# Performance work log

Hardware: AMD Instinct MI355X
Metric: run time of the kernel (lower is better)

## Reference

```python
import math
import jax, jax.numpy as jnp
import numpy as np

B, S, HID, NH = 8, 512, 1024, 16
D = HID // NH          # head dim = 64
SPAN = 512             # att_span = max_relative_positions = max_position_embeddings


def _linear(x, W, b):
    # torch nn.Linear: y = x @ W.T + b, W is [out, in]
    return jnp.einsum('...i,oi->...o', x, W) + b


def _heads(x):
    # [B, S, HID] -> [B, NH, S, D]
    b, s, _ = x.shape
    return x.reshape(b, s, NH, D).transpose(0, 2, 1, 3)


def setup_inputs() -> dict:
    key = jax.random.key(0)
    ks = jax.random.split(key, 16)
    f = lambda i, shape, sc=1.0: jax.random.normal(ks[i], shape, dtype=jnp.float32) * sc
    return {
        'q': f(0, (B, S, HID)),
        'k': f(1, (B, S, HID)),
        'v': f(2, (B, S, HID)),
        'attention_mask': jnp.tril(jnp.ones((S, S), dtype=bool))[None, None],  # causal [1,1,S,S]
        'Wq': f(3, (HID, HID), 0.02), 'bq': jnp.zeros((HID,), jnp.float32),
        'Wk': f(4, (HID, HID), 0.02), 'bk': jnp.zeros((HID,), jnp.float32),
        'Wv': f(5, (HID, HID), 0.02), 'bv': jnp.zeros((HID,), jnp.float32),
        'Wpk': f(6, (HID, HID), 0.02), 'bpk': jnp.zeros((HID,), jnp.float32),
        'Wpq': f(7, (HID, HID), 0.02), 'bpq': jnp.zeros((HID,), jnp.float32),
        'rel_emb': f(8, (2 * SPAN, HID), 0.02),
    }


def reference(q, k, v, attention_mask, Wq, bq, Wk, bk, Wv, bv, Wpk, bpk, Wpq, bpq, rel_emb):
    scale_factor = 3  # 1 (content) + c2p + p2c
    scale = 1.0 / math.sqrt(D * scale_factor)

    ql = _heads(_linear(q, Wq, bq))   # [B,NH,S,D]
    kl = _heads(_linear(k, Wk, bk))
    vl = _heads(_linear(v, Wv, bv))

    # content-to-content scores
    scores = jnp.einsum('bhqd,bhkd->bhqk', ql, kl) * scale

    # relative positions (no bucketing since position_buckets = -1)
    rel = jnp.arange(S)[:, None] - jnp.arange(S)[None, :]          # [S,S]
    c2p_pos = jnp.clip(rel + SPAN, 0, 2 * SPAN - 1)
    p2c_pos = jnp.clip(-rel + SPAN, 0, 2 * SPAN - 1)

    # projected relative-position embeddings -> [NH, 2*SPAN, D]
    pk = _linear(rel_emb, Wpk, bpk).reshape(2 * SPAN, NH, D).transpose(1, 0, 2)
    pq = _linear(rel_emb, Wpq, bpq).reshape(2 * SPAN, NH, D).transpose(1, 0, 2)

    # content-to-position: out[b,h,q,k] = (q . pos_key)[b,h,q, c2p_pos[q,k]]
    c2p = jnp.einsum('bhqd,hjd->bhqj', ql, pk) * scale             # [B,NH,S,2*SPAN]
    c2p = jnp.take_along_axis(c2p, jnp.broadcast_to(c2p_pos[None, None], (B, NH, S, S)), axis=-1)

    # position-to-content: gathered[b,h,k,q] = (k . pos_query)[b,h,k, p2c_pos[k,q]], then transpose
    p2c = jnp.einsum('bhkd,hjd->bhkj', kl, pq) * scale             # [B,NH,S,2*SPAN]
    p2c = jnp.take_along_axis(p2c, jnp.broadcast_to(p2c_pos[None, None], (B, NH, S, S)), axis=-1)

    scores = scores + c2p + jnp.swapaxes(p2c, -1, -2)
    # subtract detached row max (as in torch: .max(...).values.detach())
    scores = scores - jax.lax.stop_gradient(scores.max(axis=-1, keepdims=True))

    # XSoftmax: masked softmax, then zero masked positions
    neg = jnp.float32(-1e30)
    probs = jax.nn.softmax(jnp.where(attention_mask, scores, neg), axis=-1)
    probs = jnp.where(attention_mask, probs, 0.0)

    ctx = jnp.einsum('bhqk,bhkd->bhqd', probs, vl)                 # [B,NH,S,D]
    return ctx.transpose(0, 2, 1, 3).reshape(B, S, HID)
```

## Files before the change

### kernel.cpp

```cpp
#include <hip/hip_runtime.h>
#include <hip/hip_bf16.h>
#include <math.h>

#define SCALE 0.07216878364870323f
#define NEG_BIG -1e30f

typedef __attribute__((ext_vector_type(8))) short bf16x8;
typedef __attribute__((ext_vector_type(4))) short bf16x4;
typedef __attribute__((ext_vector_type(4))) float f32x4;
#define MFMA_BF16 __builtin_amdgcn_mfma_f32_16x16x32_bf16

#define BARX()   asm volatile("s_barrier" ::: "memory")
#define VMCNT2() asm volatile("s_waitcnt vmcnt(2)" ::: "memory")
#define VMCNT0() asm volatile("s_waitcnt vmcnt(0)" ::: "memory")

static __device__ __forceinline__ float bf2f(__hip_bfloat16 x) { return __bfloat162float(x); }
static __device__ __forceinline__ __hip_bfloat16 f2bf(float x) { return __float2bfloat16(x); }
static __device__ __forceinline__ short f2bs(float x) {
  union { __hip_bfloat16 b; short s; } u; u.b = __float2bfloat16(x); return u.s;
}
static __device__ __forceinline__ float s2f(short v) {
  union { float f; unsigned u; } x; x.u = ((unsigned)(unsigned short)v) << 16; return x.f;
}
static __device__ __forceinline__ bf16x4 cvt4(float4 f) {
  bf16x4 r; r[0] = f2bs(f.x); r[1] = f2bs(f.y); r[2] = f2bs(f.z); r[3] = f2bs(f.w);
  return r;
}
static __device__ __forceinline__ bf16x8 ldg8(const __hip_bfloat16* p) {
  return *(const bf16x8*)p;
}
static __device__ __forceinline__ void gl_lds16(const __hip_bfloat16* g, __hip_bfloat16* l) {
  __builtin_amdgcn_global_load_lds(
      (const __attribute__((address_space(1))) void*)g,
      (__attribute__((address_space(3))) void*)l, 16, 0, 0);
}

struct CvtJob { const float* src; __hip_bfloat16* dst; int n4; };
struct CvtArgs { CvtJob j[9]; };

__global__ __launch_bounds__(256) void cvt_kernel(CvtArgs a) {
  const CvtJob jb = a.j[blockIdx.y];
  const float4* s = (const float4*)jb.src;
  bf16x4* d = (bf16x4*)jb.dst;
  const int stride = gridDim.x * 256;
  for (int i = blockIdx.x * 256 + threadIdx.x; i < jb.n4; i += stride)
    d[i] = cvt4(s[i]);
}

struct Gemm { const __hip_bfloat16* A; const __hip_bfloat16* W;
              const float* bias; __hip_bfloat16* out; int mode; int mBits; int nBlk;
              float oscale; };
struct ProjArgs { Gemm g[5]; };

static __device__ __forceinline__ void stage_half(const __hip_bfloat16* gtile,
                                                  __hip_bfloat16* ltile,
                                                  int half, int wave, int lane) {
  const int r = lane >> 3;
  const int chunk = (lane & 7) ^ r;
#pragma unroll
  for (int c = 0; c < 2; c++) {
    const int rowbase = half * 128 + c * 64 + wave * 8;
    gl_lds16(gtile + (size_t)(rowbase + r) * 1024 + chunk * 8,
             ltile + (size_t)rowbase * 64);
  }
}

__global__ __launch_bounds__(512, 2) void proj_kernel(ProjArgs pa) {
  const Gemm g = pa.g[blockIdx.y];
  if ((int)blockIdx.x >= g.nBlk) return;
  __shared__ __hip_bfloat16 As[2][256][64];
  __shared__ __hip_bfloat16 Ws[2][256][64];

  const int bid = blockIdx.x;
  const int m0 = (bid & ((1 << g.mBits) - 1)) * 256;
  const int n0 = (bid >> g.mBits) * 256;
  const int tid = threadIdx.x;
  const int wave = tid >> 6, lane = tid & 63;
  const int q16 = lane >> 4, l16 = lane & 15;
  const int wr = wave >> 2, wc = wave & 3;
  const int l7 = l16 & 7;

  const __hip_bfloat16* Ag = g.A + (size_t)m0 * 1024;
  const __hip_bfloat16* Wg = g.W + (size_t)n0 * 1024;

  f32x4 acc[8][4] = {};

  stage_half(Ag, &As[0][0][0], 0, wave, lane);
  stage_half(Ag, &As[0][0][0], 1, wave, lane);
  stage_half(Wg, &Ws[0][0][0], 0, wave, lane);
  stage_half(Wg, &Ws[0][0][0], 1, wave, lane);
  stage_half(Ag + 64, &As[1][0][0], 0, wave, lane);
  VMCNT2();
  BARX();

  for (int t = 0; t < 16; ++t) {
    const int cur = t & 1;
    const __hip_bfloat16* Ac = &As[cur][0][0];
    const __hip_bfloat16* Wc = &Ws[cur][0][0];
    __hip_bfloat16* An = &As[cur ^ 1][0][0];
    __hip_bfloat16* Wn = &Ws[cur ^ 1][0][0];
    const __hip_bfloat16* gAn = Ag + (size_t)(t + 1) * 64;
    const __hip_bfloat16* gWn = Wg + (size_t)(t + 1) * 64;
    const bool pf = (t + 1 < 16);

#pragma unroll
    for (int kh = 0; kh < 2; kh++) {
      const int csw = ((kh * 4 + q16) ^ l7) * 8;
      bf16x8 bw[4];
#pragma unroll
      for (int ni = 0; ni < 4; ni++)
        bw[ni] = *(const bf16x8*)(Wc + (size_t)(wc * 64 + ni * 16 + l16) * 64 + csw);
#pragma unroll
      for (int mh = 0; mh < 2; mh++) {
        bf16x8 af[4];
#pragma unroll
        for (int mi = 0; mi < 4; mi++)
          af[mi] = *(const bf16x8*)(Ac + (size_t)(wr * 128 + mh * 64 + mi * 16 + l16) * 64 + csw);
        const int ph = kh * 2 + mh;
        if (pf) {
          if (ph == 0)      stage_half(gAn, An, 1, wave, lane);
          else if (ph == 1) stage_half(gWn, Wn, 0, wave, lane);
          else if (ph == 2) stage_half(gWn, Wn, 1, wave, lane);
        }
        __builtin_amdgcn_s_setprio(1);
#pragma unroll
        for (int ni = 0; ni < 4; ni++)
#pragma unroll
          for (int mi = 0; mi < 4; mi++)
            acc[mh * 4 + mi][ni] =
                MFMA_BF16(af[mi], bw[ni], acc[mh * 4 + mi][ni], 0, 0, 0);
        __builtin_amdgcn_s_setprio(0);
      }
    }
    BARX();
    if (t + 2 < 16) {
      stage_half(Ag + (size_t)(t + 2) * 64, &As[cur][0][0], 0, wave, lane);
      VMCNT2();
    } else {
      VMCNT0();
    }
    BARX();
  }

#pragma unroll
  for (int ni = 0; ni < 4; ni++) {
    const int n = n0 + wc * 64 + ni * 16 + l16;
#pragma unroll
    for (int mi = 0; mi < 8; mi++) {
#pragma unroll
      for (int rr = 0; rr < 4; rr++) {
        const int m = m0 + wr * 128 + mi * 16 + q16 * 4 + rr;
        float val = acc[mi][ni][rr];
        size_t oidx;
        if (g.mode == 0) {
          val = (val + g.bias[n]) * g.oscale;
          const int b = m >> 9, s = m & 511;
          const int h = n >> 6, d = n & 63;
          oidx = ((size_t)((b * 16 + h) * 512 + s)) * 64 + d;
        } else if (g.mode == 1) {
          val = (val + g.bias[m]) * g.oscale;
          const int b = n >> 9, s = n & 511;
          const int h = m >> 6, d = m & 63;
          oidx = ((size_t)((b * 16 + h) * 64 + d)) * 512 + s;
        } else {
          val = (val + g.bias[n]) * g.oscale;
          const int h = n >> 6, d = n & 63;
          oidx = ((size_t)(h * 512 + m)) * 64 + d;
        }
        g.out[oidx] = f2bf(val);
      }
    }
  }
}

__global__ __launch_bounds__(256) void attn_kernel(
    const __hip_bfloat16* __restrict__ ql,
    const __hip_bfloat16* __restrict__ kl,
    const __hip_bfloat16* __restrict__ vlT,
    const __hip_bfloat16* __restrict__ pk,
    const __hip_bfloat16* __restrict__ pq,
    float* __restrict__ out)
{
  __shared__ __align__(16) __hip_bfloat16 pool[2][64][72];
  __shared__ __align__(16) __hip_bfloat16 pqs[2][32][72];
  __shared__ __align__(16) float qkbuf[32][36];
  __shared__ __align__(16) __hip_bfloat16 cpb[2][32][68];
  __shared__ __align__(16) __hip_bfloat16 pT[64][36];
  __shared__ __align__(16) __hip_bfloat16 ptile[32][40];
  __shared__ __align__(16) __hip_bfloat16 vt[64][40];
  __shared__ float mred[32];
  __shared__ float rsum[32];

  const int bid = blockIdx.x;
  const int qt = 15 - (bid >> 7);
  const int bh = bid & 127;
  const int h = bh & 15, b = bh >> 4;
  const int q0 = qt * 32;

  const __hip_bfloat16* qlp = ql + (size_t)bh * 512 * 64;
  const __hip_bfloat16* klp = kl + (size_t)bh * 512 * 64;
  const __hip_bfloat16* vtp = vlT + (size_t)bh * 64 * 512;
  const __hip_bfloat16* pkp = pk + (size_t)h * 512 * 64;
  const __hip_bfloat16* pqp = pq + (size_t)h * 512 * 64;

  const int tid = threadIdx.x, wave = tid >> 6, lane = tid & 63;
  const int q16 = lane >> 4, l16 = lane & 15;
  const int wr = wave & 1, wc = wave >> 1;

  bf16x8 qlB[2][2];
#pragma unroll
  for (int ksi = 0; ksi < 2; ksi++)
#pragma unroll
    for (int bq = 0; bq < 2; bq++)
      qlB[ksi][bq] = ldg8(qlp + (size_t)(q0 + bq * 16 + l16) * 64 + ksi * 32 + q16 * 8);

  {
    int4 z = {0, 0, 0, 0};
    *(int4*)(&pqs[1][tid >> 3][(tid & 7) * 8]) = z;
  }

  const int kEnd = q0 + 32;
  const int nIter = kEnd >> 5;

  const int sr = tid >> 3, sseg = tid & 7;
  const int vr = tid >> 2, vs = tid & 3;
  int4 rKv, rPKv, rPQv, rVt;
  {
    rKv  = ((const int4*)(klp + (size_t)(q0 + sr) * 64))[sseg];
    rPKv = ((const int4*)(pkp + (size_t)(0 + sr) * 64))[sseg];
    rPQv = ((const int4*)(pqp + (size_t)(0 + sr) * 64))[sseg];
    rVt  = ((const int4*)(vtp + (size_t)vr * 512 + q0))[vs];
  }

  const int aq = tid >> 3;
  const int kb = (tid & 7) * 4;
  float m_old = -INFINITY, s_part = 0.f;
  f32x4 octx[2] = {};

  for (int it = 0; it < nIter; ++it) {
    const int k0 = q0 - it * 32;
    const int par = it & 1;
    *(int4*)(&pool[par][sr][sseg * 8])      = rKv;
    *(int4*)(&pool[par][32 + sr][sseg * 8]) = rPKv;
    *(int4*)(&pqs[par][sr][sseg * 8])       = rPQv;
    if (it + 1 < nIter) {
      const int k0n = k0 - 32, jbn = (it + 1) * 32;
      rKv  = ((const int4*)(klp + (size_t)(k0n + sr) * 64))[sseg];
      rPKv = ((const int4*)(pkp + (size_t)(jbn + sr) * 64))[sseg];
      rPQv = ((const int4*)(pqp + (size_t)(jbn + sr) * 64))[sseg];
    }
    __syncthreads();

    const int arb = (wave == 1) ? 32 : 0;
    f32x4 a4[2][2] = {};
    __builtin_amdgcn_s_setprio(1);
#pragma unroll
    for (int ksi = 0; ksi < 2; ksi++) {
      const int ko = ksi * 32 + q16 * 8;
      bf16x8 Af0 = *(const bf16x8*)(&pool[par][arb + l16][ko]);
      bf16x8 Af1 = *(const bf16x8*)(&pool[par][arb + 16 + l16][ko]);
      bf16x8 Bf0, Bf1;
      if (wave < 2) {
        Bf0 = qlB[ksi][0];
        Bf1 = qlB[ksi][1];
      } else {
        const int ps = (wave == 2) ? (par ^ 1) : par;
        Bf0 = *(const bf16x8*)(&pqs[ps][l16][ko]);
        Bf1 = *(const bf16x8*)(&pqs[ps][16 + l16][ko]);
      }
      a4[0][0] = MFMA_BF16(Af0, Bf0, a4[0][0], 0, 0, 0);
      a4[0][1] = MFMA_BF16(Af0, Bf1, a4[0][1], 0, 0, 0);
      a4[1][0] = MFMA_BF16(Af1, Bf0, a4[1][0], 0, 0, 0);
      a4[1][1] = MFMA_BF16(Af1, Bf1, a4[1][1], 0, 0, 0);
    }
    __builtin_amdgcn_s_setprio(0);
    if (wave == 0) {
#pragma unroll
      for (int a = 0; a < 2; a++)
#pragma unroll
        for (int bq = 0; bq < 2; bq++)
          *(f32x4*)(&qkbuf[bq * 16 + l16][a * 16 + q16 * 4]) = a4[a][bq];
    } else if (wave == 1) {
#pragma unroll
      for (int a = 0; a < 2; a++)
#pragma unroll
        for (int bq = 0; bq < 2; bq++) {
          bf16x4 v;
#pragma unroll
          for (int r = 0; r < 4; r++) v[r] = f2bs(a4[a][bq][r]);
          const int q = bq * 16 + l16, jr = a * 16 + q16 * 4;
          *(bf16x4*)(&cpb[par][q][32 + jr]) = v;
          *(bf16x4*)(&cpb[par ^ 1][q][jr]) = v;
        }
    } else {
      const int rb = (wave == 3) ? 32 : 0;
#pragma unroll
      for (int a = 0; a < 2; a++)
#pragma unroll
        for (int bq = 0; bq < 2; bq++) {
          bf16x4 v;
#pragma unroll
          for (int r = 0; r < 4; r++) v[r] = f2bs(a4[a][bq][r]);
          *(bf16x4*)(&pT[rb + bq * 16 + l16][a * 16 + q16 * 4]) = v;
        }
    }
    __syncthreads();

    {
      const f32x4 qk4 = *(const f32x4*)(&qkbuf[aq][kb]);
      float v[4];
      float tmax = -INFINITY;
#pragma unroll
      for (int j = 0; j < 4; j++) {
        const int dlt = aq - (kb + j);
        v[j] = qk4[j] + bf2f(cpb[par][aq][dlt + 32]) + bf2f(pT[dlt + 32][kb + j]);
        if ((it == 0) && (dlt < 0)) v[j] = -INFINITY;
        else tmax = fmaxf(tmax, v[j]);
      }
      tmax = fmaxf(tmax, __shfl_xor(tmax, 1));
      tmax = fmaxf(tmax, __shfl_xor(tmax, 2));
      tmax = fmaxf(tmax, __shfl_xor(tmax, 4));
      const float m_new = fmaxf(m_old, tmax);
      const float f = __expf(m_old - m_new);
      bf16x4 pv4;
      float psum = 0.f;
#pragma unroll
      for (int j = 0; j < 4; j++) {
        const float p = __expf(v[j] - m_new);
        pv4[j] = f2bs(p);
        psum += p;
      }
      s_part = s_part * f + psum;
      m_old = m_new;
      *(bf16x4*)(&ptile[aq][kb]) = pv4;
      if ((tid & 7) == 0) mred[aq] = f;
    }
    {
      *(int4*)(&vt[vr][vs * 8]) = rVt;
      if (it + 1 < nIter)
        rVt = ((const int4*)(vtp + (size_t)vr * 512 + (k0 - 32)))[vs];
    }
    __syncthreads();

    {
      float fr[4];
#pragma unroll
      for (int rr = 0; rr < 4; rr++) fr[rr] = mred[wr * 16 + q16 * 4 + rr];
      bf16x8 af = *(const bf16x8*)(&ptile[wr * 16 + l16][q16 * 8]);
      __builtin_amdgcn_s_setprio(1);
#pragma unroll
      for (int cs = 0; cs < 2; cs++) {
        bf16x8 bv = *(const bf16x8*)(&vt[wc * 32 + cs * 16 + l16][q16 * 8]);
        f32x4 c = octx[cs];
#pragma unroll
        for (int rr = 0; rr < 4; rr++) c[rr] *= fr[rr];
        octx[cs] = MFMA_BF16(af, bv, c, 0, 0, 0);
      }
      __builtin_amdgcn_s_setprio(0);
    }
  }

  {
    float s = s_part;
    s += __shfl_xor(s, 1);
    s += __shfl_xor(s, 2);
    s += __shfl_xor(s, 4);
    if ((tid & 7) == 0) rsum[aq] = s;
  }
  __syncthreads();

  for (int cs = 0; cs < 2; cs++) {
    const int d = wc * 32 + cs * 16 + l16;
    for (int rr = 0; rr < 4; rr++) {
      const int qh = wr * 16 + q16 * 4 + rr;
      const float val = octx[cs][rr] / rsum[qh];
      out[((size_t)(b * 512 + q0 + qh)) * 1024 + h * 64 + d] = val;
    }
  }
}

extern "C" void kernel_launch(void* const* d_in, const int* in_sizes, int n_in,
                              void* d_out, int out_size, void* d_ws, size_t ws_size,
                              hipStream_t stream) {
  const float* q   = (const float*)d_in[0];
  const float* k   = (const float*)d_in[1];
  const float* v   = (const float*)d_in[2];
  const float* Wq  = (const float*)d_in[4];
  const float* bq  = (const float*)d_in[5];
  const float* Wk  = (const float*)d_in[6];
  const float* bk  = (const float*)d_in[7];
  const float* Wv  = (const float*)d_in[8];
  const float* bv  = (const float*)d_in[9];
  const float* Wpk = (const float*)d_in[10];
  const float* bpk = (const float*)d_in[11];
  const float* Wpq = (const float*)d_in[12];
  const float* bpq = (const float*)d_in[13];
  const float* rel = (const float*)d_in[14];
  float* out = (float*)d_out;

  char* ws = (char*)d_ws;
  const size_t MB = 1u << 20;
  __hip_bfloat16* bqi  = (__hip_bfloat16*)(ws);
  __hip_bfloat16* bki  = (__hip_bfloat16*)(ws + 8 * MB);
  __hip_bfloat16* bvi  = (__hip_bfloat16*)(ws + 16 * MB);
  __hip_bfloat16* bWq  = (__hip_bfloat16*)(ws + 24 * MB);
  __hip_bfloat16* bWk  = (__hip_bfloat16*)(ws + 26 * MB);
  __hip_bfloat16* bWv  = (__hip_bfloat16*)(ws + 28 * MB);
  __hip_bfloat16* bWpk = (__hip_bfloat16*)(ws + 30 * MB);
  __hip_bfloat16* bWpq = (__hip_bfloat16*)(ws + 32 * MB);
  __hip_bfloat16* brel = (__hip_bfloat16*)(ws + 34 * MB);
  __hip_bfloat16* wql  = (__hip_bfloat16*)(ws + 35 * MB);
  __hip_bfloat16* wkl  = (__hip_bfloat16*)(ws + 43 * MB);
  __hip_bfloat16* wvlT = (__hip_bfloat16*)(ws + 51 * MB);
  __hip_bfloat16* wpk  = (__hip_bfloat16*)(ws + 59 * MB);
  __hip_bfloat16* wpq  = (__hip_bfloat16*)(ws + 60 * MB);

  CvtArgs ca;
  ca.j[0] = { q,   bqi,  4194304 / 4 };
  ca.j[1] = { k,   bki,  4194304 / 4 };
  ca.j[2] = { v,   bvi,  4194304 / 4 };
  ca.j[3] = { Wq,  bWq,  1048576 / 4 };
  ca.j[4] = { Wk,  bWk,  1048576 / 4 };
  ca.j[5] = { Wv,  bWv,  1048576 / 4 };
  ca.j[6] = { Wpk, bWpk, 1048576 / 4 };
  ca.j[7] = { Wpq, bWpq, 1048576 / 4 };
  ca.j[8] = { rel + (size_t)512 * 1024, brel, 524288 / 4 };
  cvt_kernel<<<dim3(1024, 9), 256, 0, stream>>>(ca);

  ProjArgs pj;
  pj.g[0] = { bqi,  bWq,  bq,  wql,  0, 4, 64, SCALE };
  pj.g[1] = { bki,  bWk,  bk,  wkl,  0, 4, 64, 1.0f };
  pj.g[2] = { bWv,  bvi,  bv,  wvlT, 1, 2, 64, 1.0f };
  pj.g[3] = { brel, bWpk, bpk, wpk,  2, 1, 8,  1.0f };
  pj.g[4] = { brel, bWpq, bpq, wpq,  2, 1, 8,  SCALE };
  proj_kernel<<<dim3(64, 5), 512, 0, stream>>>(pj);

  attn_kernel<<<2048, 256, 0, stream>>>(wql, wkl, wvlT, wpk, wpq, out);
}
```

Before: 231.5 us.

## Restructure projection GEMM to 4-stage pipeline with 32-wide K slices

```diff
diff --git a/kernel.cpp b/kernel.cpp
--- a/kernel.cpp
+++ b/kernel.cpp
@@ -11,8 +11,11 @@
 #define MFMA_BF16 __builtin_amdgcn_mfma_f32_16x16x32_bf16
 
 #define BARX()   asm volatile("s_barrier" ::: "memory")
-#define VMCNT2() asm volatile("s_waitcnt vmcnt(2)" ::: "memory")
+#define VMCNT8() asm volatile("s_waitcnt vmcnt(8)" ::: "memory")
+#define VMCNT4() asm volatile("s_waitcnt vmcnt(4)" ::: "memory")
 #define VMCNT0() asm volatile("s_waitcnt vmcnt(0)" ::: "memory")
+#define LGKM0()  do { asm volatile("s_waitcnt lgkmcnt(0)" ::: "memory"); \
+                      __builtin_amdgcn_sched_barrier(0); } while (0)
 
 static __device__ __forceinline__ float bf2f(__hip_bfloat16 x) { return __bfloat162float(x); }
 static __device__ __forceinline__ __hip_bfloat16 f2bf(float x) { return __float2bfloat16(x); }
@@ -52,24 +55,24 @@
               float oscale; };
 struct ProjArgs { Gemm g[5]; };
 
-static __device__ __forceinline__ void stage_half(const __hip_bfloat16* gtile,
-                                                  __hip_bfloat16* ltile,
-                                                  int half, int wave, int lane) {
-  const int r = lane >> 3;
-  const int chunk = (lane & 7) ^ r;
+static __device__ __forceinline__ void stage32(const __hip_bfloat16* gpanel,
+                                               __hip_bfloat16* lslot,
+                                               int tt, int wave, int lane) {
+  const int rsub = lane >> 2;
+  const int chunk = lane & 3;
 #pragma unroll
   for (int c = 0; c < 2; c++) {
-    const int rowbase = half * 128 + c * 64 + wave * 8;
-    gl_lds16(gtile + (size_t)(rowbase + r) * 1024 + chunk * 8,
-             ltile + (size_t)rowbase * 64);
+    const int row = c * 128 + wave * 16 + rsub;
+    gl_lds16(gpanel + (size_t)row * 1024 + tt * 32 + chunk * 8,
+             lslot + (size_t)(c * 128 + wave * 16) * 32);
   }
 }
 
 __global__ __launch_bounds__(512, 2) void proj_kernel(ProjArgs pa) {
   const Gemm g = pa.g[blockIdx.y];
   if ((int)blockIdx.x >= g.nBlk) return;
-  __shared__ __hip_bfloat16 As[2][256][64];
-  __shared__ __hip_bfloat16 Ws[2][256][64];
+  __shared__ __hip_bfloat16 As[4][256][32];
+  __shared__ __hip_bfloat16 Ws[4][256][32];
 
   const int bid = blockIdx.x;
   const int m0 = (bid & ((1 << g.mBits) - 1)) * 256;
@@ -78,68 +81,71 @@
   const int wave = tid >> 6, lane = tid & 63;
   const int q16 = lane >> 4, l16 = lane & 15;
   const int wr = wave >> 2, wc = wave & 3;
-  const int l7 = l16 & 7;
 
   const __hip_bfloat16* Ag = g.A + (size_t)m0 * 1024;
   const __hip_bfloat16* Wg = g.W + (size_t)n0 * 1024;
 
   f32x4 acc[8][4] = {};
 
-  stage_half(Ag, &As[0][0][0], 0, wave, lane);
-  stage_half(Ag, &As[0][0][0], 1, wave, lane);
-  stage_half(Wg, &Ws[0][0][0], 0, wave, lane);
-  stage_half(Wg, &Ws[0][0][0], 1, wave, lane);
-  stage_half(Ag + 64, &As[1][0][0], 0, wave, lane);
-  VMCNT2();
+  stage32(Ag, &As[0][0][0], 0, wave, lane);
+  stage32(Wg, &Ws[0][0][0], 0, wave, lane);
+  stage32(Ag, &As[1][0][0], 1, wave, lane);
+  stage32(Wg, &Ws[1][0][0], 1, wave, lane);
+  stage32(Ag, &As[2][0][0], 2, wave, lane);
+  stage32(Wg, &Ws[2][0][0], 2, wave, lane);
+  VMCNT8();
   BARX();
 
-  for (int t = 0; t < 16; ++t) {
-    const int cur = t & 1;
-    const __hip_bfloat16* Ac = &As[cur][0][0];
-    const __hip_bfloat16* Wc = &Ws[cur][0][0];
-    __hip_bfloat16* An = &As[cur ^ 1][0][0];
-    __hip_bfloat16* Wn = &Ws[cur ^ 1][0][0];
-    const __hip_bfloat16* gAn = Ag + (size_t)(t + 1) * 64;
-    const __hip_bfloat16* gWn = Wg + (size_t)(t + 1) * 64;
-    const bool pf = (t + 1 < 16);
-
-#pragma unroll
-    for (int kh = 0; kh < 2; kh++) {
-      const int csw = ((kh * 4 + q16) ^ l7) * 8;
-      bf16x8 bw[4];
-#pragma unroll
-      for (int ni = 0; ni < 4; ni++)
-        bw[ni] = *(const bf16x8*)(Wc + (size_t)(wc * 64 + ni * 16 + l16) * 64 + csw);
-#pragma unroll
-      for (int mh = 0; mh < 2; mh++) {
-        bf16x8 af[4];
-#pragma unroll
-        for (int mi = 0; mi < 4; mi++)
-          af[mi] = *(const bf16x8*)(Ac + (size_t)(wr * 128 + mh * 64 + mi * 16 + l16) * 64 + csw);
-        const int ph = kh * 2 + mh;
-        if (pf) {
-          if (ph == 0)      stage_half(gAn, An, 1, wave, lane);
-          else if (ph == 1) stage_half(gWn, Wn, 0, wave, lane);
-          else if (ph == 2) stage_half(gWn, Wn, 1, wave, lane);
-        }
-        __builtin_amdgcn_s_setprio(1);
-#pragma unroll
-        for (int ni = 0; ni < 4; ni++)
-#pragma unroll
-          for (int mi = 0; mi < 4; mi++)
-            acc[mh * 4 + mi][ni] =
-                MFMA_BF16(af[mi], bw[ni], acc[mh * 4 + mi][ni], 0, 0, 0);
-        __builtin_amdgcn_s_setprio(0);
-      }
-    }
+  const int rA0 = (wr * 128 + l16) * 32 + q16 * 8;
+  const int rA1 = (wr * 128 + 64 + l16) * 32 + q16 * 8;
+  const int rW  = (wc * 64 + l16) * 32 + q16 * 8;
+
+  for (int t = 0; t < 32; ++t) {
+    const int s = t & 3;
+    const __hip_bfloat16* Ac = &As[s][0][0];
+    const __hip_bfloat16* Wc = &Ws[s][0][0];
+    const bool pf = (t + 3 < 32);
+    const int sn = (t + 3) & 3;
+
+    bf16x8 bw[4], af[4];
+#pragma unroll
+    for (int ni = 0; ni < 4; ni++)
+      bw[ni] = *(const bf16x8*)(Wc + rW + ni * 16 * 32);
+#pragma unroll
+    for (int mi = 0; mi < 4; mi++)
+      af[mi] = *(const bf16x8*)(Ac + rA0 + mi * 16 * 32);
+    if (pf) stage32(Ag, &As[sn][0][0], t + 3, wave, lane);
     BARX();
-    if (t + 2 < 16) {
-      stage_half(Ag + (size_t)(t + 2) * 64, &As[cur][0][0], 0, wave, lane);
-      VMCNT2();
-    } else {
-      VMCNT0();
-    }
+    LGKM0();
+    __builtin_amdgcn_s_setprio(1);
+#pragma unroll
+    for (int ni = 0; ni < 4; ni++)
+#pragma unroll
+      for (int mi = 0; mi < 4; mi++)
+        acc[mi][ni] = MFMA_BF16(af[mi], bw[ni], acc[mi][ni], 0, 0, 0);
+    __builtin_amdgcn_s_setprio(0);
     BARX();
+
+#pragma unroll
+    for (int mi = 0; mi < 4; mi++)
+      af[mi] = *(const bf16x8*)(Ac + rA1 + mi * 16 * 32);
+    if (pf) stage32(Wg, &Ws[sn][0][0], t + 3, wave, lane);
+    BARX();
+    LGKM0();
+    __builtin_amdgcn_s_setprio(1);
+#pragma unroll
+    for (int ni = 0; ni < 4; ni++)
+#pragma unroll
+      for (int mi = 0; mi < 4; mi++)
+        acc[4 + mi][ni] = MFMA_BF16(af[mi], bw[ni], acc[4 + mi][ni], 0, 0, 0);
+    __builtin_amdgcn_s_setprio(0);
+
+    if (t < 31) {
+      if (t <= 28)      VMCNT8();
+      else if (t == 29) VMCNT4();
+      else              VMCNT0();
+      BARX();
+    }
   }
 
 #pragma unroll
```

Measured after the change: 234.7 us. About the same (+1.4%).

## Fuse fp32-to-bf16 activation conversion into projection GEMM tile loading

Applied to the files above, without the earlier changes.

```diff
diff --git a/kernel.cpp b/kernel.cpp
--- a/kernel.cpp
+++ b/kernel.cpp
@@ -10,10 +10,6 @@
 typedef __attribute__((ext_vector_type(4))) float f32x4;
 #define MFMA_BF16 __builtin_amdgcn_mfma_f32_16x16x32_bf16
 
-#define BARX()   asm volatile("s_barrier" ::: "memory")
-#define VMCNT2() asm volatile("s_waitcnt vmcnt(2)" ::: "memory")
-#define VMCNT0() asm volatile("s_waitcnt vmcnt(0)" ::: "memory")
-
 static __device__ __forceinline__ float bf2f(__hip_bfloat16 x) { return __bfloat162float(x); }
 static __device__ __forceinline__ __hip_bfloat16 f2bf(float x) { return __float2bfloat16(x); }
 static __device__ __forceinline__ short f2bs(float x) {
@@ -36,7 +32,7 @@
 }
 
 struct CvtJob { const float* src; __hip_bfloat16* dst; int n4; };
-struct CvtArgs { CvtJob j[9]; };
+struct CvtArgs { CvtJob j[6]; };
 
 __global__ __launch_bounds__(256) void cvt_kernel(CvtArgs a) {
   const CvtJob jb = a.j[blockIdx.y];
@@ -47,21 +43,45 @@
     d[i] = cvt4(s[i]);
 }
 
-struct Gemm { const __hip_bfloat16* A; const __hip_bfloat16* W;
-              const float* bias; __hip_bfloat16* out; int mode; int mBits; int nBlk;
-              float oscale; };
+struct Gemm { const void* A; const void* W; const float* bias; __hip_bfloat16* out;
+              int mode; int mBits; int nBlk; float oscale; int aF32; int wF32; };
 struct ProjArgs { Gemm g[5]; };
 
-static __device__ __forceinline__ void stage_half(const __hip_bfloat16* gtile,
-                                                  __hip_bfloat16* ltile,
-                                                  int half, int wave, int lane) {
+static __device__ __forceinline__ void stage_bf16(const __hip_bfloat16* gpanel, int kcol,
+                                                  __hip_bfloat16* ltile, int wave, int lane) {
   const int r = lane >> 3;
   const int chunk = (lane & 7) ^ r;
 #pragma unroll
-  for (int c = 0; c < 2; c++) {
-    const int rowbase = half * 128 + c * 64 + wave * 8;
-    gl_lds16(gtile + (size_t)(rowbase + r) * 1024 + chunk * 8,
+  for (int hc = 0; hc < 4; hc++) {
+    const int rowbase = hc * 64 + wave * 8;
+    gl_lds16(gpanel + (size_t)(rowbase + r) * 1024 + kcol + chunk * 8,
              ltile + (size_t)rowbase * 64);
+  }
+}
+
+static __device__ __forceinline__ void load_f32(const float* gpanel, int kcol,
+                                                float4* st, int wave, int lane) {
+  const int r = lane >> 3;
+  const int chunk = (lane & 7) ^ r;
+#pragma unroll
+  for (int hc = 0; hc < 4; hc++) {
+    const int row = hc * 64 + wave * 8 + r;
+    const float* src = gpanel + (size_t)row * 1024 + kcol + chunk * 8;
+    st[hc * 2 + 0] = *(const float4*)(src);
+    st[hc * 2 + 1] = *(const float4*)(src + 4);
+  }
+}
+
+static __device__ __forceinline__ void write_f32(__hip_bfloat16* ltile,
+                                                 const float4* st, int wave, int lane) {
+#pragma unroll
+  for (int hc = 0; hc < 4; hc++) {
+    const int rowbase = hc * 64 + wave * 8;
+    const float4 lo = st[hc * 2 + 0], hi = st[hc * 2 + 1];
+    bf16x8 v;
+    v[0] = f2bs(lo.x); v[1] = f2bs(lo.y); v[2] = f2bs(lo.z); v[3] = f2bs(lo.w);
+    v[4] = f2bs(hi.x); v[5] = f2bs(hi.y); v[6] = f2bs(hi.z); v[7] = f2bs(hi.w);
+    *(bf16x8*)(ltile + (size_t)rowbase * 64 + lane * 8) = v;
   }
 }
 
@@ -80,29 +100,49 @@
   const int wr = wave >> 2, wc = wave & 3;
   const int l7 = l16 & 7;
 
-  const __hip_bfloat16* Ag = g.A + (size_t)m0 * 1024;
-  const __hip_bfloat16* Wg = g.W + (size_t)n0 * 1024;
+  const bool af32 = (g.aF32 != 0), wf32 = (g.wF32 != 0);
+  const float* Ag32 = (const float*)g.A + (size_t)m0 * 1024;
+  const float* Wg32 = (const float*)g.W + (size_t)n0 * 1024;
+  const __hip_bfloat16* Ag16 = (const __hip_bfloat16*)g.A + (size_t)m0 * 1024;
+  const __hip_bfloat16* Wg16 = (const __hip_bfloat16*)g.W + (size_t)n0 * 1024;
 
   f32x4 acc[8][4] = {};
-
-  stage_half(Ag, &As[0][0][0], 0, wave, lane);
-  stage_half(Ag, &As[0][0][0], 1, wave, lane);
-  stage_half(Wg, &Ws[0][0][0], 0, wave, lane);
-  stage_half(Wg, &Ws[0][0][0], 1, wave, lane);
-  stage_half(Ag + 64, &As[1][0][0], 0, wave, lane);
-  VMCNT2();
-  BARX();
+  float4 stF[8];
+
+  if (af32) {
+    load_f32(Ag32, 0, stF, wave, lane);
+    write_f32(&As[0][0][0], stF, wave, lane);
+    load_f32(Ag32, 64, stF, wave, lane);
+  } else {
+    stage_bf16(Ag16, 0, &As[0][0][0], wave, lane);
+  }
+  if (wf32) {
+    load_f32(Wg32, 0, stF, wave, lane);
+    write_f32(&Ws[0][0][0], stF, wave, lane);
+    load_f32(Wg32, 64, stF, wave, lane);
+  } else {
+    stage_bf16(Wg16, 0, &Ws[0][0][0], wave, lane);
+  }
 
   for (int t = 0; t < 16; ++t) {
-    const int cur = t & 1;
-    const __hip_bfloat16* Ac = &As[cur][0][0];
-    const __hip_bfloat16* Wc = &Ws[cur][0][0];
-    __hip_bfloat16* An = &As[cur ^ 1][0][0];
-    __hip_bfloat16* Wn = &Ws[cur ^ 1][0][0];
-    const __hip_bfloat16* gAn = Ag + (size_t)(t + 1) * 64;
-    const __hip_bfloat16* gWn = Wg + (size_t)(t + 1) * 64;
-    const bool pf = (t + 1 < 16);
-
+    __syncthreads();
+    if (t + 1 < 16) {
+      const int kn = (t + 1) * 64;
+      if (af32) {
+        write_f32(&As[(t + 1) & 1][0][0], stF, wave, lane);
+        if (t + 2 < 16) load_f32(Ag32, (t + 2) * 64, stF, wave, lane);
+      } else {
+        stage_bf16(Ag16, kn, &As[(t + 1) & 1][0][0], wave, lane);
+      }
+      if (wf32) {
+        write_f32(&Ws[(t + 1) & 1][0][0], stF, wave, lane);
+        if (t + 2 < 16) load_f32(Wg32, (t + 2) * 64, stF, wave, lane);
+      } else {
+        stage_bf16(Wg16, kn, &Ws[(t + 1) & 1][0][0], wave, lane);
+      }
+    }
+    const __hip_bfloat16* Ac = &As[t & 1][0][0];
+    const __hip_bfloat16* Wc = &Ws[t & 1][0][0];
 #pragma unroll
     for (int kh = 0; kh < 2; kh++) {
       const int csw = ((kh * 4 + q16) ^ l7) * 8;
@@ -116,12 +156,6 @@
 #pragma unroll
         for (int mi = 0; mi < 4; mi++)
           af[mi] = *(const bf16x8*)(Ac + (size_t)(wr * 128 + mh * 64 + mi * 16 + l16) * 64 + csw);
-        const int ph = kh * 2 + mh;
-        if (pf) {
-          if (ph == 0)      stage_half(gAn, An, 1, wave, lane);
-          else if (ph == 1) stage_half(gWn, Wn, 0, wave, lane);
-          else if (ph == 2) stage_half(gWn, Wn, 1, wave, lane);
-        }
         __builtin_amdgcn_s_setprio(1);
 #pragma unroll
         for (int ni = 0; ni < 4; ni++)
@@ -132,14 +166,6 @@
         __builtin_amdgcn_s_setprio(0);
       }
     }
-    BARX();
-    if (t + 2 < 16) {
-      stage_half(Ag + (size_t)(t + 2) * 64, &As[cur][0][0], 0, wave, lane);
-      VMCNT2();
-    } else {
-      VMCNT0();
-    }
-    BARX();
   }
 
 #pragma unroll
@@ -400,9 +426,6 @@
 
   char* ws = (char*)d_ws;
   const size_t MB = 1u << 20;
-  __hip_bfloat16* bqi  = (__hip_bfloat16*)(ws);
-  __hip_bfloat16* bki  = (__hip_bfloat16*)(ws + 8 * MB);
-  __hip_bfloat16* bvi  = (__hip_bfloat16*)(ws + 16 * MB);
   __hip_bfloat16* bWq  = (__hip_bfloat16*)(ws + 24 * MB);
   __hip_bfloat16* bWk  = (__hip_bfloat16*)(ws + 26 * MB);
   __hip_bfloat16* bWv  = (__hip_bfloat16*)(ws + 28 * MB);
@@ -416,23 +439,20 @@
   __hip_bfloat16* wpq  = (__hip_bfloat16*)(ws + 60 * MB);
 
   CvtArgs ca;
-  ca.j[0] = { q,   bqi,  4194304 / 4 };
-  ca.j[1] = { k,   bki,  4194304 / 4 };
-  ca.j[2] = { v,   bvi,  4194304 / 4 };
-  ca.j[3] = { Wq,  bWq,  1048576 / 4 };
-  ca.j[4] = { Wk,  bWk,  1048576 / 4 };
-  ca.j[5] = { Wv,  bWv,  1048576 / 4 };
-  ca.j[6] = { Wpk, bWpk, 1048576 / 4 };
-  ca.j[7] = { Wpq, bWpq, 1048576 / 4 };
-  ca.j[8] = { rel + (size_t)512 * 1024, brel, 524288 / 4 };
-  cvt_kernel<<<dim3(1024, 9), 256, 0, stream>>>(ca);
+  ca.j[0] = { Wq,  bWq,  1048576 / 4 };
+  ca.j[1] = { Wk,  bWk,  1048576 / 4 };
+  ca.j[2] = { Wv,  bWv,  1048576 / 4 };
+  ca.j[3] = { Wpk, bWpk, 1048576 / 4 };
+  ca.j[4] = { Wpq, bWpq, 1048576 / 4 };
+  ca.j[5] = { rel + (size_t)512 * 1024, brel, 524288 / 4 };
+  cvt_kernel<<<dim3(256, 6), 256, 0, stream>>>(ca);
 
   ProjArgs pj;
-  pj.g[0] = { bqi,  bWq,  bq,  wql,  0, 4, 64, SCALE };
-  pj.g[1] = { bki,  bWk,  bk,  wkl,  0, 4, 64, 1.0f };
-  pj.g[2] = { bWv,  bvi,  bv,  wvlT, 1, 2, 64, 1.0f };
-  pj.g[3] = { brel, bWpk, bpk, wpk,  2, 1, 8,  1.0f };
-  pj.g[4] = { brel, bWpq, bpq, wpq,  2, 1, 8,  SCALE };
+  pj.g[0] = { q,    bWq,  bq,  wql,  0, 4, 64, SCALE, 1, 0 };
+  pj.g[1] = { k,    bWk,  bk,  wkl,  0, 4, 64, 1.0f,  1, 0 };
+  pj.g[2] = { bWv,  v,    bv,  wvlT, 1, 2, 64, 1.0f,  0, 1 };
+  pj.g[3] = { brel, bWpk, bpk, wpk,  2, 1, 8,  1.0f,  0, 0 };
+  pj.g[4] = { brel, bWpq, bpq, wpq,  2, 1, 8,  SCALE, 0, 0 };
   proj_kernel<<<dim3(64, 5), 512, 0, stream>>>(pj);
 
   attn_kernel<<<2048, 256, 0, stream>>>(wql, wkl, wvlT, wpk, wpq, out);
```

New measurement: 243.4 us. 5.1% more time.

## Restructure projection GEMM main loop into barrier-synchronized 8-phase ping-pong schedule

Applied to the files above, without the earlier changes.

```diff
diff --git a/kernel.cpp b/kernel.cpp
--- a/kernel.cpp
+++ b/kernel.cpp
@@ -11,8 +11,9 @@
 #define MFMA_BF16 __builtin_amdgcn_mfma_f32_16x16x32_bf16
 
 #define BARX()   asm volatile("s_barrier" ::: "memory")
-#define VMCNT2() asm volatile("s_waitcnt vmcnt(2)" ::: "memory")
 #define VMCNT0() asm volatile("s_waitcnt vmcnt(0)" ::: "memory")
+#define LGKM0()  do { asm volatile("s_waitcnt lgkmcnt(0)" ::: "memory"); \
+                      __builtin_amdgcn_sched_barrier(0); } while (0)
 
 static __device__ __forceinline__ float bf2f(__hip_bfloat16 x) { return __bfloat162float(x); }
 static __device__ __forceinline__ __hip_bfloat16 f2bf(float x) { return __float2bfloat16(x); }
@@ -89,57 +90,62 @@
   stage_half(Ag, &As[0][0][0], 1, wave, lane);
   stage_half(Wg, &Ws[0][0][0], 0, wave, lane);
   stage_half(Wg, &Ws[0][0][0], 1, wave, lane);
-  stage_half(Ag + 64, &As[1][0][0], 0, wave, lane);
-  VMCNT2();
+  VMCNT0();
   BARX();
 
   for (int t = 0; t < 16; ++t) {
-    const int cur = t & 1;
-    const __hip_bfloat16* Ac = &As[cur][0][0];
-    const __hip_bfloat16* Wc = &Ws[cur][0][0];
-    __hip_bfloat16* An = &As[cur ^ 1][0][0];
-    __hip_bfloat16* Wn = &Ws[cur ^ 1][0][0];
-    const __hip_bfloat16* gAn = Ag + (size_t)(t + 1) * 64;
-    const __hip_bfloat16* gWn = Wg + (size_t)(t + 1) * 64;
+    const int sl = t & 1, sn = sl ^ 1;
+    const __hip_bfloat16* Ac = &As[sl][0][0];
+    const __hip_bfloat16* Wc = &Ws[sl][0][0];
     const bool pf = (t + 1 < 16);
-
+    const __hip_bfloat16* gA1 = Ag + (size_t)(t + 1) * 64;
+    const __hip_bfloat16* gW1 = Wg + (size_t)(t + 1) * 64;
+
+    bf16x8 bw[4], af[4];
 #pragma unroll
     for (int kh = 0; kh < 2; kh++) {
       const int csw = ((kh * 4 + q16) ^ l7) * 8;
-      bf16x8 bw[4];
+
 #pragma unroll
       for (int ni = 0; ni < 4; ni++)
         bw[ni] = *(const bf16x8*)(Wc + (size_t)(wc * 64 + ni * 16 + l16) * 64 + csw);
 #pragma unroll
-      for (int mh = 0; mh < 2; mh++) {
-        bf16x8 af[4];
+      for (int mi = 0; mi < 4; mi++)
+        af[mi] = *(const bf16x8*)(Ac + (size_t)(wr * 128 + mi * 16 + l16) * 64 + csw);
+      if (pf) {
+        if (kh == 0) stage_half(gA1, &As[sn][0][0], 0, wave, lane);
+        else         stage_half(gW1, &Ws[sn][0][0], 0, wave, lane);
+      }
+      BARX();
+      LGKM0();
+      __builtin_amdgcn_s_setprio(1);
+#pragma unroll
+      for (int ni = 0; ni < 4; ni++)
 #pragma unroll
         for (int mi = 0; mi < 4; mi++)
-          af[mi] = *(const bf16x8*)(Ac + (size_t)(wr * 128 + mh * 64 + mi * 16 + l16) * 64 + csw);
-        const int ph = kh * 2 + mh;
-        if (pf) {
-          if (ph == 0)      stage_half(gAn, An, 1, wave, lane);
-          else if (ph == 1) stage_half(gWn, Wn, 0, wave, lane);
-          else if (ph == 2) stage_half(gWn, Wn, 1, wave, lane);
-        }
-        __builtin_amdgcn_s_setprio(1);
-#pragma unroll
-        for (int ni = 0; ni < 4; ni++)
-#pragma unroll
-          for (int mi = 0; mi < 4; mi++)
-            acc[mh * 4 + mi][ni] =
-                MFMA_BF16(af[mi], bw[ni], acc[mh * 4 + mi][ni], 0, 0, 0);
-        __builtin_amdgcn_s_setprio(0);
-      }
-    }
-    BARX();
-    if (t + 2 < 16) {
-      stage_half(Ag + (size_t)(t + 2) * 64, &As[cur][0][0], 0, wave, lane);
-      VMCNT2();
-    } else {
-      VMCNT0();
-    }
-    BARX();
+          acc[mi][ni] = MFMA_BF16(af[mi], bw[ni], acc[mi][ni], 0, 0, 0);
+      __builtin_amdgcn_s_setprio(0);
+      BARX();
+
+#pragma unroll
+      for (int mi = 0; mi < 4; mi++)
+        af[mi] = *(const bf16x8*)(Ac + (size_t)(wr * 128 + 64 + mi * 16 + l16) * 64 + csw);
+      if (pf) {
+        if (kh == 0) stage_half(gA1, &As[sn][0][0], 1, wave, lane);
+        else         stage_half(gW1, &Ws[sn][0][0], 1, wave, lane);
+      }
+      BARX();
+      LGKM0();
+      __builtin_amdgcn_s_setprio(1);
+#pragma unroll
+      for (int ni = 0; ni < 4; ni++)
+#pragma unroll
+        for (int mi = 0; mi < 4; mi++)
+          acc[4 + mi][ni] = MFMA_BF16(af[mi], bw[ni], acc[4 + mi][ni], 0, 0, 0);
+      __builtin_amdgcn_s_setprio(0);
+      if (kh == 1 && pf) VMCNT0();
+      BARX();
+    }
   }
 
 #pragma unroll
```

Result: no change. 231.4 us (-0.1%).
